# Optimization experiments

Hardware: AMD Instinct MI355X
Metric: run time of the kernel (lower is better)

Reference implementation:

```python
import jax, jax.numpy as jnp
import numpy as np

# ---- static hash-grid config (mirrors init_kwargs) ----
RANGE = 1.0
DIM = 3
N_LEVELS = 16
F_PER_LEVEL = 2
LOG2_HASHMAP = 15
HASHMAP_SIZE = 1 << LOG2_HASHMAP
BASE_RES = 16
FINEST_RES = 512
RANK = 4
PRIMES = np.array([1, 2654435761, 805459861], dtype=np.uint32)


def _resolutions():
    # N_l = floor(base * b^l), b = exp((ln(Nmax)-ln(Nmin))/(L-1))  (Instant-NGP eq. 2-3)
    b = np.exp((np.log(FINEST_RES) - np.log(BASE_RES)) / (N_LEVELS - 1))
    return np.floor(BASE_RES * b ** np.arange(N_LEVELS)).astype(np.float32)


def setup_inputs() -> dict:
    key = jax.random.key(0)
    k1, k2, k3 = jax.random.split(key, 3)
    x = jax.random.uniform(k1, (524288, DIM), dtype=jnp.float32)  # in [-range, range]
    # LoRA factors; small init like hash-grid tables (~1e-2 scale)
    table_A = jax.random.normal(k2, (N_LEVELS, HASHMAP_SIZE, RANK), dtype=jnp.float32) * 1e-2
    table_B = jax.random.normal(k3, (N_LEVELS, RANK, F_PER_LEVEL), dtype=jnp.float32) * 1e-1
    return {"x": x, "table_A": table_A, "table_B": table_B}


def reference(x, table_A, table_B):
    # wrapper: normalize to [0,1]
    xn = (x + RANGE) / (2.0 * RANGE)                         # [N,3]
    res = jnp.asarray(_resolutions())                        # [L]

    # materialize tiny per-level tables from LoRA factors: [L, S, F]
    tables = jnp.einsum('lsr,lrf->lsf', table_A, table_B)

    xl = xn[None, :, :] * res[:, None, None]                 # [L,N,3]
    xf = jnp.floor(xl)
    w = xl - xf                                              # [L,N,3] trilinear weights
    xi = xf.astype(jnp.uint32)                               # [L,N,3]

    # 2^3 corner offsets
    corners = jnp.array([[(c >> d) & 1 for d in range(DIM)] for c in range(2 ** DIM)],
                        dtype=jnp.uint32)                    # [8,3]

    pos = xi[:, :, None, :] + corners[None, None, :, :]      # [L,N,8,3]
    primes = jnp.asarray(PRIMES)
    h = (pos[..., 0] * primes[0]) ^ (pos[..., 1] * primes[1]) ^ (pos[..., 2] * primes[2])
    idx = (h & jnp.uint32(HASHMAP_SIZE - 1)).astype(jnp.int32)  # [L,N,8]

    # per-level gather: [L,N,8,F]
    feats = jax.vmap(lambda t, i: t[i])(tables, idx)

    # trilinear weights per corner: prod over dims of (w or 1-w)
    wc = jnp.prod(jnp.where(corners[None, None, :, :] == 1,
                            w[:, :, None, :], 1.0 - w[:, :, None, :]), axis=-1)  # [L,N,8]

    out_l = jnp.sum(feats * wc[..., None], axis=2)           # [L,N,F]
    out = jnp.transpose(out_l, (1, 0, 2)).reshape(x.shape[0], N_LEVELS * F_PER_LEVEL)
    return out.astype(jnp.float32)
```

## Files before the change

### kernel.cpp

```cpp
#include <hip/hip_runtime.h>
#include <hip/hip_fp16.h>
#include <math.h>
#include <stdint.h>
#include <stddef.h>

#define NLEVELS 16
#define HSIZE   32768
#define LOGH    15
#define RANKK   4
#define PRIME1  2654435761u
#define PRIME2  805459861u

#define BLK  1024
#define PPB  32768

struct ResArr { float v[NLEVELS]; };

__global__ void build_tables_k(const float* __restrict__ A, const float* __restrict__ B,
                               uint32_t* __restrict__ T) {
    int i = blockIdx.x * blockDim.x + threadIdx.x;
    if (i >= NLEVELS * HSIZE) return;
    int l = i >> LOGH;
    const float4 a = *reinterpret_cast<const float4*>(A + (size_t)i * RANKK);
    const float* b = B + l * (RANKK * 2);
    float f0 = a.x * b[0] + a.y * b[2] + a.z * b[4] + a.w * b[6];
    float f1 = a.x * b[1] + a.y * b[3] + a.z * b[5] + a.w * b[7];
    __half2 h = __floats2half2_rn(f0, f1);
    T[i] = *reinterpret_cast<uint32_t*>(&h);
}

__global__ __launch_bounds__(BLK) __attribute__((amdgpu_waves_per_eu(4, 4)))
void encode_level_k(const float* __restrict__ x, const uint32_t* __restrict__ T,
                    void* __restrict__ dst_base, int nPoints, int directOut,
                    ResArr res) {
    __shared__ uint32_t lds[HSIZE];
    const int l     = blockIdx.x & (NLEVELS - 1);
    const int chunk = blockIdx.x >> 4;
    const int t     = threadIdx.x;

    {
        const uint4* Tl4 = reinterpret_cast<const uint4*>(T + (size_t)l * HSIZE);
        uint4* lds4 = reinterpret_cast<uint4*>(lds);
#pragma unroll
        for (int k = 0; k < HSIZE / 4 / BLK; ++k)
            lds4[k * BLK + t] = Tl4[k * BLK + t];
    }
    __syncthreads();

    const float r = res.v[l];
    const int base = chunk * PPB;
    __half2* outTh = reinterpret_cast<__half2*>(dst_base);
    float*   outF  = reinterpret_cast<float*>(dst_base);

    for (int k = 0; k < PPB; k += 2 * BLK) {
        int   n[2];
        bool  ok[2];
        float acc0[2], acc1[2];
        float w2v[2], w2a_[2];
        float wxy00[2], wxy10[2], wxy01[2], wxy11[2];
        uint32_t hx0[2], hx1[2], hy0[2], hy1[2], hz0[2], hz1[2];

#pragma unroll
        for (int u = 0; u < 2; ++u) {
            n[u]  = base + k + u * BLK + t;
            ok[u] = (n[u] < nPoints);
            int m = ok[u] ? n[u] : 0;
            float xn0 = (x[3 * m + 0] + 1.0f) * 0.5f;
            float xn1 = (x[3 * m + 1] + 1.0f) * 0.5f;
            float xn2 = (x[3 * m + 2] + 1.0f) * 0.5f;
            float xl0 = xn0 * r, xl1 = xn1 * r, xl2 = xn2 * r;
            float fl0 = floorf(xl0), fl1 = floorf(xl1), fl2 = floorf(xl2);
            float w0 = xl0 - fl0, w1 = xl1 - fl1, w2 = xl2 - fl2;
            uint32_t i0 = (uint32_t)fl0, i1 = (uint32_t)fl1, i2 = (uint32_t)fl2;

            hx0[u] = i0;          hx1[u] = i0 + 1u;
            hy0[u] = i1 * PRIME1; hy1[u] = hy0[u] + PRIME1;
            hz0[u] = i2 * PRIME2; hz1[u] = hz0[u] + PRIME2;

            float w0a = 1.0f - w0, w1a = 1.0f - w1;
            w2v[u] = w2; w2a_[u] = 1.0f - w2;
            wxy00[u] = w0a * w1a; wxy10[u] = w0 * w1a;
            wxy01[u] = w0a * w1;  wxy11[u] = w0 * w1;
            acc0[u] = 0.0f; acc1[u] = 0.0f;
        }

#pragma unroll
        for (int c = 0; c < 8; ++c) {
#pragma unroll
            for (int u = 0; u < 2; ++u) {
                uint32_t h = ((c & 1) ? hx1[u] : hx0[u]) ^ ((c & 2) ? hy1[u] : hy0[u])
                           ^ ((c & 4) ? hz1[u] : hz0[u]);
                uint32_t pk = lds[h & (HSIZE - 1)];
                __half2 h2 = *reinterpret_cast<__half2*>(&pk);
                float2 f = __half22float2(h2);
                float wxy = (c & 2) ? ((c & 1) ? wxy11[u] : wxy01[u])
                                    : ((c & 1) ? wxy10[u] : wxy00[u]);
                float wc = wxy * ((c & 4) ? w2v[u] : w2a_[u]);
                acc0[u] = fmaf(f.x, wc, acc0[u]);
                acc1[u] = fmaf(f.y, wc, acc1[u]);
            }
        }

#pragma unroll
        for (int u = 0; u < 2; ++u) {
            if (!ok[u]) continue;
            if (directOut) {
                *reinterpret_cast<float2*>(outF + (size_t)n[u] * 32 + 2 * l) =
                    make_float2(acc0[u], acc1[u]);
            } else {
                outTh[(size_t)l * nPoints + n[u]] = __floats2half2_rn(acc0[u], acc1[u]);
            }
        }
    }
}

__global__ __launch_bounds__(256)
void merge_k(const __half2* __restrict__ outTh, float* __restrict__ out, int nPoints) {
    int p2 = blockIdx.x * blockDim.x + threadIdx.x;
    int n0 = 2 * p2;
    if (n0 >= nPoints) return;
    bool has1 = (n0 + 1) < nPoints;

    float4 oA[8], oB[8];
#pragma unroll
    for (int q = 0; q < 8; ++q) {
        __half2 s0[2], s1[2];
        *reinterpret_cast<uint2*>(s0) =
            *reinterpret_cast<const uint2*>(outTh + (size_t)(2 * q) * nPoints + n0);
        *reinterpret_cast<uint2*>(s1) =
            *reinterpret_cast<const uint2*>(outTh + (size_t)(2 * q + 1) * nPoints + n0);
        float2 a0 = __half22float2(s0[0]), a1 = __half22float2(s0[1]);
        float2 b0 = __half22float2(s1[0]), b1 = __half22float2(s1[1]);
        oA[q] = make_float4(a0.x, a0.y, b0.x, b0.y);
        oB[q] = make_float4(a1.x, a1.y, b1.x, b1.y);
    }
    float4* dstA = reinterpret_cast<float4*>(out + (size_t)n0 * 32);
#pragma unroll
    for (int q = 0; q < 8; ++q) dstA[q] = oA[q];
    if (has1) {
        float4* dstB = reinterpret_cast<float4*>(out + (size_t)(n0 + 1) * 32);
#pragma unroll
        for (int q = 0; q < 8; ++q) dstB[q] = oB[q];
    }
}

__global__ void encode_fallback_k(const float* __restrict__ x, const float* __restrict__ A,
                                  const float* __restrict__ B, float* __restrict__ out,
                                  int nPoints, ResArr res) {
    int n = blockIdx.x * blockDim.x + threadIdx.x;
    if (n >= nPoints) return;
    float xn0 = (x[3 * n + 0] + 1.0f) * 0.5f;
    float xn1 = (x[3 * n + 1] + 1.0f) * 0.5f;
    float xn2 = (x[3 * n + 2] + 1.0f) * 0.5f;
    for (int l = 0; l < NLEVELS; ++l) {
        float r = res.v[l];
        float xl0 = xn0 * r, xl1 = xn1 * r, xl2 = xn2 * r;
        float fl0 = floorf(xl0), fl1 = floorf(xl1), fl2 = floorf(xl2);
        float w0 = xl0 - fl0, w1 = xl1 - fl1, w2 = xl2 - fl2;
        uint32_t i0 = (uint32_t)fl0, i1 = (uint32_t)fl1, i2 = (uint32_t)fl2;
        uint32_t hx0 = i0,          hx1 = i0 + 1u;
        uint32_t hy0 = i1 * PRIME1, hy1 = hy0 + PRIME1;
        uint32_t hz0 = i2 * PRIME2, hz1 = hz0 + PRIME2;
        float w0a = 1.0f - w0, w1a = 1.0f - w1, w2a = 1.0f - w2;
        float wxy00 = w0a * w1a, wxy10 = w0 * w1a, wxy01 = w0a * w1, wxy11 = w0 * w1;
        const float* b = B + l * 8;
        float b00 = b[0], b01 = b[1], b10 = b[2], b11 = b[3];
        float b20 = b[4], b21 = b[5], b30 = b[6], b31 = b[7];
        float acc0 = 0.0f, acc1 = 0.0f;
#pragma unroll
        for (int c = 0; c < 8; ++c) {
            uint32_t h = ((c & 1) ? hx1 : hx0) ^ ((c & 2) ? hy1 : hy0) ^ ((c & 4) ? hz1 : hz0);
            uint32_t idx = h & (HSIZE - 1);
            float4 a = *reinterpret_cast<const float4*>(A + ((size_t)l * HSIZE + idx) * RANKK);
            float fe0 = a.x * b00 + a.y * b10 + a.z * b20 + a.w * b30;
            float fe1 = a.x * b01 + a.y * b11 + a.z * b21 + a.w * b31;
            float wxy = (c & 2) ? ((c & 1) ? wxy11 : wxy01) : ((c & 1) ? wxy10 : wxy00);
            float wc = wxy * ((c & 4) ? w2 : w2a);
            acc0 = fmaf(fe0, wc, acc0);
            acc1 = fmaf(fe1, wc, acc1);
        }
        out[(size_t)n * 32 + 2 * l + 0] = acc0;
        out[(size_t)n * 32 + 2 * l + 1] = acc1;
    }
}

extern "C" void kernel_launch(void* const* d_in, const int* in_sizes, int n_in,
                              void* d_out, int out_size, void* d_ws, size_t ws_size,
                              hipStream_t stream) {
    const float* x = (const float*)d_in[0];
    const float* A = (const float*)d_in[1];
    const float* B = (const float*)d_in[2];
    float* out = (float*)d_out;
    int nPoints = in_sizes[0] / 3;

    ResArr ra;
    {
        double b = exp((log(512.0) - log(16.0)) / 15.0);
        for (int l = 0; l < NLEVELS; ++l)
            ra.v[l] = (float)floor(16.0 * pow(b, (double)l));
    }

    const size_t tblBytes  = (size_t)NLEVELS * HSIZE * sizeof(uint32_t);
    const size_t outTBytes = (size_t)NLEVELS * (size_t)nPoints * sizeof(__half2);

    if (ws_size >= tblBytes) {
        uint32_t* T = (uint32_t*)d_ws;
        int nb1 = (NLEVELS * HSIZE + 255) / 256;
        build_tables_k<<<nb1, 256, 0, stream>>>(A, B, T);
        int chunks = (nPoints + PPB - 1) / PPB;
        if (ws_size >= tblBytes + outTBytes) {
            void* outT = (void*)((char*)d_ws + tblBytes);
            encode_level_k<<<chunks * NLEVELS, BLK, 0, stream>>>(x, T, outT, nPoints, 0, ra);
            int pairs = (nPoints + 1) / 2;
            merge_k<<<(pairs + 255) / 256, 256, 0, stream>>>((const __half2*)outT, out, nPoints);
        } else {
            encode_level_k<<<chunks * NLEVELS, BLK, 0, stream>>>(x, T, (void*)out, nPoints, 1, ra);
        }
    } else {
        encode_fallback_k<<<(nPoints + 255) / 256, 256, 0, stream>>>(x, A, B, out, nPoints, ra);
    }
}
```

Baseline: 133.3 us.

## Write encoder output directly, drop fp16 staging and merge pass

Drops the half-precision level-major staging buffer and the separate merge kernel. Each level block now writes float2 results straight into the final point-major output with strided 8-byte stores. Blocks are ordered level-major, so all chunks of one level run together, and the chunk size is halved to double the block count. This removes one kernel launch and a full write-then-read pass over the intermediate buffer, in exchange for uncoalesced strided global stores and twice as many per-block LDS table loads.

```diff
diff --git a/kernel.cpp b/kernel.cpp
--- a/kernel.cpp
+++ b/kernel.cpp
@@ -12,7 +12,7 @@
 #define PRIME2  805459861u
 
 #define BLK  1024
-#define PPB  32768
+#define PPB  16384
 
 struct ResArr { float v[NLEVELS]; };
 
@@ -30,12 +30,11 @@
 }
 
 __global__ __launch_bounds__(BLK) __attribute__((amdgpu_waves_per_eu(4, 4)))
-void encode_level_k(const float* __restrict__ x, const uint32_t* __restrict__ T,
-                    void* __restrict__ dst_base, int nPoints, int directOut,
-                    ResArr res) {
+void encode_direct_k(const float* __restrict__ x, const uint32_t* __restrict__ T,
+                     float* __restrict__ out, int nPoints, int nChunks, ResArr res) {
     __shared__ uint32_t lds[HSIZE];
-    const int l     = blockIdx.x & (NLEVELS - 1);
-    const int chunk = blockIdx.x >> 4;
+    const int chunk = blockIdx.x % nChunks;
+    const int l     = blockIdx.x / nChunks;
     const int t     = threadIdx.x;
 
     {
@@ -49,8 +48,7 @@
 
     const float r = res.v[l];
     const int base = chunk * PPB;
-    __half2* outTh = reinterpret_cast<__half2*>(dst_base);
-    float*   outF  = reinterpret_cast<float*>(dst_base);
+    float2* out2 = reinterpret_cast<float2*>(out);
 
     for (int k = 0; k < PPB; k += 2 * BLK) {
         int   n[2];
@@ -104,43 +102,8 @@
 #pragma unroll
         for (int u = 0; u < 2; ++u) {
             if (!ok[u]) continue;
-            if (directOut) {
-                *reinterpret_cast<float2*>(outF + (size_t)n[u] * 32 + 2 * l) =
-                    make_float2(acc0[u], acc1[u]);
-            } else {
-                outTh[(size_t)l * nPoints + n[u]] = __floats2half2_rn(acc0[u], acc1[u]);
-            }
+            out2[(size_t)n[u] * NLEVELS + l] = make_float2(acc0[u], acc1[u]);
         }
-    }
-}
-
-__global__ __launch_bounds__(256)
-void merge_k(const __half2* __restrict__ outTh, float* __restrict__ out, int nPoints) {
-    int p2 = blockIdx.x * blockDim.x + threadIdx.x;
-    int n0 = 2 * p2;
-    if (n0 >= nPoints) return;
-    bool has1 = (n0 + 1) < nPoints;
-
-    float4 oA[8], oB[8];
-#pragma unroll
-    for (int q = 0; q < 8; ++q) {
-        __half2 s0[2], s1[2];
-        *reinterpret_cast<uint2*>(s0) =
-            *reinterpret_cast<const uint2*>(outTh + (size_t)(2 * q) * nPoints + n0);
-        *reinterpret_cast<uint2*>(s1) =
-            *reinterpret_cast<const uint2*>(outTh + (size_t)(2 * q + 1) * nPoints + n0);
-        float2 a0 = __half22float2(s0[0]), a1 = __half22float2(s0[1]);
-        float2 b0 = __half22float2(s1[0]), b1 = __half22float2(s1[1]);
-        oA[q] = make_float4(a0.x, a0.y, b0.x, b0.y);
-        oB[q] = make_float4(a1.x, a1.y, b1.x, b1.y);
-    }
-    float4* dstA = reinterpret_cast<float4*>(out + (size_t)n0 * 32);
-#pragma unroll
-    for (int q = 0; q < 8; ++q) dstA[q] = oA[q];
-    if (has1) {
-        float4* dstB = reinterpret_cast<float4*>(out + (size_t)(n0 + 1) * 32);
-#pragma unroll
-        for (int q = 0; q < 8; ++q) dstB[q] = oB[q];
     }
 }
 
@@ -200,22 +163,14 @@
             ra.v[l] = (float)floor(16.0 * pow(b, (double)l));
     }
 
-    const size_t tblBytes  = (size_t)NLEVELS * HSIZE * sizeof(uint32_t);
-    const size_t outTBytes = (size_t)NLEVELS * (size_t)nPoints * sizeof(__half2);
+    const size_t tblBytes = (size_t)NLEVELS * HSIZE * sizeof(uint32_t);
 
     if (ws_size >= tblBytes) {
         uint32_t* T = (uint32_t*)d_ws;
         int nb1 = (NLEVELS * HSIZE + 255) / 256;
         build_tables_k<<<nb1, 256, 0, stream>>>(A, B, T);
         int chunks = (nPoints + PPB - 1) / PPB;
-        if (ws_size >= tblBytes + outTBytes) {
-            void* outT = (void*)((char*)d_ws + tblBytes);
-            encode_level_k<<<chunks * NLEVELS, BLK, 0, stream>>>(x, T, outT, nPoints, 0, ra);
-            int pairs = (nPoints + 1) / 2;
-            merge_k<<<(pairs + 255) / 256, 256, 0, stream>>>((const __half2*)outT, out, nPoints);
-        } else {
-            encode_level_k<<<chunks * NLEVELS, BLK, 0, stream>>>(x, T, (void*)out, nPoints, 1, ra);
-        }
+        encode_direct_k<<<chunks * NLEVELS, BLK, 0, stream>>>(x, T, out, nPoints, chunks, ra);
     } else {
         encode_fallback_k<<<(nPoints + 255) / 256, 256, 0, stream>>>(x, A, B, out, nPoints, ra);
     }
```

Result: no change. 131.0 us (-1.8%).
